# Performance work log

Measured on AMD Instinct MI355X. Metric: run time of the kernel, lower is better.

## Reference

```python
import jax, jax.numpy as jnp
import numpy as np

G = 8            # n_group
C = 256          # input_dim / channels
N_MEM = C // G   # 32
ALPHA = 0.4      # w_alpha
EPS = 1e-5
SLOPE = 0.01     # LeakyReLU negative slope


def _lrelu(x):
    return jnp.where(x >= 0, x, SLOPE * x)


def _mlp(x, ws, bs):
    # torch nn.Linear convention: y = x @ W.T + b; lrelu on all but last layer
    n = len(ws)
    for i in range(n):
        x = x @ ws[i].T + bs[i]
        if i < n - 1:
            x = _lrelu(x)
    return x


def _wct(c_A, s_B, mask, ct_ws, ct_bs, mu_ws, mu_bs):
    B, Cc, H, W = c_A.shape
    n_mem = Cc // G
    # style -> per-group coloring matrices  (Get.coloring, vectorized over groups)
    s_CT = _mlp(s_B.reshape(B * G, n_mem), ct_ws, ct_bs).reshape(B, G, n_mem, n_mem)
    D = jnp.sqrt(jnp.sum(s_CT ** 2, axis=2, keepdims=True))        # [B,G,1,n_mem]
    U = s_CT / D                                                    # column-normalized
    UDU = jnp.einsum('bgij,bgkj->bgik', s_CT, U)                    # [B,G,n_mem,n_mem]
    # torch.cat(U_arr, dim=0) is group-major: index g*B+b
    eigen_s = jnp.transpose(U, (1, 0, 2, 3)).reshape(G * B, n_mem, n_mem)
    X = jnp.tile(UDU.reshape(B, Cc, n_mem), (1, 1, G)) * mask       # [B,C,C]
    s_mu = _mlp(s_B, mu_ws, mu_bs)[:, :, None, None]                # [B,C,1,1]
    # per-group covariance of mean-centered content
    c_g = jnp.transpose(c_A, (1, 0, 2, 3)).reshape(G, n_mem, B * H * W)
    c_g = c_g - jnp.mean(c_g, axis=2, keepdims=True)
    cov_c = jnp.einsum('gin,gjn->gij', c_g, c_g) / (B * H * W - 1) \
        + EPS * jnp.eye(n_mem, dtype=c_A.dtype)
    # centered content, reinterpreted as [B, C, H*W] (matches torch view/permute)
    whitend = jnp.transpose(c_g.reshape(Cc, B, H * W), (1, 0, 2))
    colored = jnp.einsum('bcd,bdn->bcn', X, whitend).reshape(B, Cc, H, W)
    out = ALPHA * (colored + s_mu) + (1.0 - ALPHA) * c_A
    return out, cov_c, eigen_s


def setup_inputs():
    key = jax.random.key(0)
    ks = jax.random.split(key, 16)
    B, H, W = 4, 128, 128
    c_A = jax.random.normal(ks[0], (B, C, H, W), dtype=jnp.float32)
    s_B = jax.random.normal(ks[1], (B, C), dtype=jnp.float32)
    # block-diagonal group mask [1, C, C]
    m = np.zeros((C, C), dtype=np.float32)
    for g in range(G):
        m[g * N_MEM:(g + 1) * N_MEM, g * N_MEM:(g + 1) * N_MEM] = 1.0
    mask = jnp.asarray(m)[None]

    def lin(k, o, i):
        return jax.random.normal(k, (o, i), dtype=jnp.float32) * (1.0 / np.sqrt(i))

    inp = {'c_A': c_A, 's_B': s_B, 'mask': mask}
    dims_ct = [(256, 32), (256, 256), (256, 256), (256, 256), (1024, 256)]
    for j, (o, i) in enumerate(dims_ct):
        inp['ct_w%d' % j] = lin(ks[2 + j], o, i)
        inp['ct_b%d' % j] = jnp.zeros((o,), dtype=jnp.float32)
    dims_mu = [(256, 256), (256, 256), (256, 256)]
    for j, (o, i) in enumerate(dims_mu):
        inp['mu_w%d' % j] = lin(ks[8 + j], o, i)
        inp['mu_b%d' % j] = jnp.zeros((o,), dtype=jnp.float32)
    return inp


def reference(c_A, s_B, mask, ct_w0, ct_b0, ct_w1, ct_b1, ct_w2, ct_b2,
              ct_w3, ct_b3, ct_w4, ct_b4, mu_w0, mu_b0, mu_w1, mu_b1,
              mu_w2, mu_b2):
    ct_ws = (ct_w0, ct_w1, ct_w2, ct_w3, ct_w4)
    ct_bs = (ct_b0, ct_b1, ct_b2, ct_b3, ct_b4)
    mu_ws = (mu_w0, mu_w1, mu_w2)
    mu_bs = (mu_b0, mu_b1, mu_b2)
    return _wct(c_A, s_B, mask, ct_ws, ct_bs, mu_ws, mu_bs)
```

## Files before the change

### kernel.cpp

```cpp
#include <hip/hip_runtime.h>
#include <hip/hip_bf16.h>

typedef __bf16 bf16x8 __attribute__((ext_vector_type(8)));
typedef float  f32x16 __attribute__((ext_vector_type(16)));

#define ALPHA_W 0.4f
#define NTOT 65536.0f

#define OUT_MAIN 16777216
#define OUT_COV  (OUT_MAIN)
#define OUT_EIG  (OUT_MAIN + 8192)

#define WS_PSXY  0
#define WS_PSX   524288
#define WS_XA    540672
#define WS_XB    548864
#define WS_MUA   557056
#define WS_MUB   558080
#define WS_SMU   559104
#define WS_CT    560128
#define WS_M     592896
#define WS_T     625664

struct LJ { const float* X; const float* W; const float* B; float* Y; int act; int out; };

__device__ __forceinline__ float lrelu(float x) { return x >= 0.f ? x : 0.01f * x; }

__device__ __forceinline__ float dotg256(const float* __restrict__ w, const float* __restrict__ x) {
    float a0 = 0.f, a1 = 0.f, a2 = 0.f, a3 = 0.f;
    #pragma unroll
    for (int i = 0; i < 256; i += 16) {
        float4 w0 = *(const float4*)(w + i);
        float4 w1 = *(const float4*)(w + i + 4);
        float4 w2 = *(const float4*)(w + i + 8);
        float4 w3 = *(const float4*)(w + i + 12);
        float4 x0 = *(const float4*)(x + i);
        float4 x1 = *(const float4*)(x + i + 4);
        float4 x2 = *(const float4*)(x + i + 8);
        float4 x3 = *(const float4*)(x + i + 12);
        a0 = fmaf(w0.x, x0.x, a0); a0 = fmaf(w0.y, x0.y, a0);
        a0 = fmaf(w0.z, x0.z, a0); a0 = fmaf(w0.w, x0.w, a0);
        a1 = fmaf(w1.x, x1.x, a1); a1 = fmaf(w1.y, x1.y, a1);
        a1 = fmaf(w1.z, x1.z, a1); a1 = fmaf(w1.w, x1.w, a1);
        a2 = fmaf(w2.x, x2.x, a2); a2 = fmaf(w2.y, x2.y, a2);
        a2 = fmaf(w2.z, x2.z, a2); a2 = fmaf(w2.w, x2.w, a2);
        a3 = fmaf(w3.x, x3.x, a3); a3 = fmaf(w3.y, x3.y, a3);
        a3 = fmaf(w3.z, x3.z, a3); a3 = fmaf(w3.w, x3.w, a3);
    }
    return (a0 + a1) + (a2 + a3);
}

__global__ __launch_bounds__(256, 2) void gram_kernel(const float* __restrict__ cA,
                                                      float* __restrict__ pSXY,
                                                      float* __restrict__ pSX) {
    int bid = blockIdx.x;
    int g = bid >> 6, slice = bid & 63;
    int tid = threadIdx.x;
    int w = tid >> 6, l = tid & 63;
    int col = l & 31, kq = l >> 5;
    int nbase = slice * 1024 + w * 256;
    int b = nbase >> 14, hw0 = nbase & 16383;
    const float* base = cA + (((size_t)(b * 256 + g * 32 + col)) << 14) + hw0 + kq * 8;
    f32x16 acc;
    #pragma unroll
    for (int r = 0; r < 16; r++) acc[r] = 0.f;
    float s0 = 0.f, s1 = 0.f;
    #pragma unroll 8
    for (int it = 0; it < 16; ++it) {
        float4 f0 = *(const float4*)(base + it * 16);
        float4 f1 = *(const float4*)(base + it * 16 + 4);
        s0 += (f0.x + f0.y) + (f0.z + f0.w);
        s1 += (f1.x + f1.y) + (f1.z + f1.w);
        bf16x8 v;
        v[0] = (__bf16)f0.x; v[1] = (__bf16)f0.y; v[2] = (__bf16)f0.z; v[3] = (__bf16)f0.w;
        v[4] = (__bf16)f1.x; v[5] = (__bf16)f1.y; v[6] = (__bf16)f1.z; v[7] = (__bf16)f1.w;
        acc = __builtin_amdgcn_mfma_f32_32x32x16_bf16(v, v, acc, 0, 0, 0);
    }
    __shared__ float red[4][1024];
    __shared__ float sxr[4][64];
    sxr[w][l] = s0 + s1;
    #pragma unroll
    for (int r = 0; r < 16; r++) {
        int i = (r & 3) + 8 * (r >> 2) + 4 * kq;
        red[w][i * 32 + col] = acc[r];
    }
    __syncthreads();
    for (int e = tid; e < 1024; e += 256)
        pSXY[(size_t)bid * 1024 + e] = red[0][e] + red[1][e] + red[2][e] + red[3][e];
    if (tid < 32) {
        float v = 0.f;
        #pragma unroll
        for (int ww = 0; ww < 4; ww++) v += sxr[ww][tid] + sxr[ww][tid + 32];
        pSX[bid * 32 + tid] = v;
    }
}

__global__ __launch_bounds__(256, 2) void lin_first(const float* __restrict__ sB,
                                                    const float* __restrict__ w0,
                                                    const float* __restrict__ b0,
                                                    float* __restrict__ XA,
                                                    const float* __restrict__ mw0,
                                                    const float* __restrict__ mb0,
                                                    float* __restrict__ MUA) {
    int bid = blockIdx.x, tid = threadIdx.x;
    if (bid < 32) {
        __shared__ float xls[32 * 36];
        #pragma unroll
        for (int c = 0; c < 4; c++) {
            int idx = c * 256 + tid;
            xls[(idx >> 5) * 36 + (idx & 31)] = sB[idx];
        }
        __syncthreads();
        int o = bid * 8 + (tid & 7), r = tid >> 3;
        const float* wr = w0 + o * 32;
        const float* xr = xls + r * 36;
        float a0 = 0.f, a1 = 0.f;
        #pragma unroll
        for (int i = 0; i < 32; i += 8) {
            float4 u0 = *(const float4*)(wr + i);
            float4 u1 = *(const float4*)(wr + i + 4);
            float4 x0 = *(const float4*)(xr + i);
            float4 x1 = *(const float4*)(xr + i + 4);
            a0 = fmaf(u0.x, x0.x, a0); a0 = fmaf(u0.y, x0.y, a0);
            a0 = fmaf(u0.z, x0.z, a0); a0 = fmaf(u0.w, x0.w, a0);
            a1 = fmaf(u1.x, x1.x, a1); a1 = fmaf(u1.y, x1.y, a1);
            a1 = fmaf(u1.z, x1.z, a1); a1 = fmaf(u1.w, x1.w, a1);
        }
        XA[r * 256 + o] = lrelu(a0 + a1 + b0[o]);
    } else {
        __shared__ float xmu[4 * 260];
        {
            int idx = tid * 4;
            float4 v = *(const float4*)(sB + idx);
            *(float4*)(xmu + (idx >> 8) * 260 + (idx & 255)) = v;
        }
        __syncthreads();
        int o = (bid - 32) * 64 + (tid & 63), r = tid >> 6;
        float v = dotg256(mw0 + (size_t)o * 256, xmu + r * 260);
        MUA[r * 256 + o] = lrelu(v + mb0[o]);
    }
}

__global__ __launch_bounds__(256, 2) void lin256(LJ a, LJ b, int nbA) {
    int bid = blockIdx.x, tid = threadIdx.x;
    __shared__ float xls[32 * 260];
    if (bid < nbA) {
        #pragma unroll
        for (int c = 0; c < 8; c++) {
            int idx = c * 1024 + tid * 4;
            float4 v = *(const float4*)(a.X + idx);
            *(float4*)(xls + (idx >> 8) * 260 + (idx & 255)) = v;
        }
        __syncthreads();
        int o = bid * 8 + (tid & 7), r = tid >> 3;
        float v = dotg256(a.W + (size_t)o * 256, xls + r * 260) + a.B[o];
        a.Y[r * a.out + o] = a.act ? lrelu(v) : v;
    } else {
        {
            int idx = tid * 4;
            float4 v = *(const float4*)(b.X + idx);
            *(float4*)(xls + (idx >> 8) * 260 + (idx & 255)) = v;
        }
        __syncthreads();
        int o = (bid - nbA) * 64 + (tid & 63), r = tid >> 6;
        float v = dotg256(b.W + (size_t)o * 256, xls + r * 260) + b.B[o];
        b.Y[r * b.out + o] = b.act ? lrelu(v) : v;
    }
}

__global__ __launch_bounds__(256, 2) void finalize(const float* __restrict__ CT,
                                                   const float* __restrict__ SMU,
                                                   const float* __restrict__ pSXY,
                                                   const float* __restrict__ pSX,
                                                   float* __restrict__ M,
                                                   float* __restrict__ T,
                                                   float* __restrict__ out) {
    int bid = blockIdx.x, t = threadIdx.x;
    __shared__ float sxg[32];
    if (bid < 32) {
        int b = bid >> 3, g = bid & 7;
        __shared__ float sct[32 * 33], uu[32 * 33], ud[32 * 33], dinv[32];
        for (int e = t; e < 1024; e += 256) sct[(e >> 5) * 33 + (e & 31)] = CT[bid * 1024 + e];
        if (t < 32) {
            float s = 0.f;
            #pragma unroll
            for (int sl = 0; sl < 64; sl++) s += pSX[(g * 64 + sl) * 32 + t];
            sxg[t] = s * (1.0f / NTOT);
        }
        __syncthreads();
        if (t < 32) {
            float s = 0.f;
            #pragma unroll
            for (int i = 0; i < 32; i++) { float v = sct[i * 33 + t]; s = fmaf(v, v, s); }
            dinv[t] = 1.0f / sqrtf(s);
        }
        __syncthreads();
        float* eig = out + OUT_EIG + (size_t)(g * 4 + b) * 1024;
        for (int e = t; e < 1024; e += 256) {
            int i = e >> 5, jj = e & 31;
            float u = sct[i * 33 + jj] * dinv[jj];
            uu[i * 33 + jj] = u;
            eig[e] = u;
        }
        __syncthreads();
        float* Mo = M + (size_t)bid * 1024;
        for (int e = t; e < 1024; e += 256) {
            int i = e >> 5, k = e & 31;
            float s = 0.f;
            #pragma unroll
            for (int jv = 0; jv < 32; jv++) s = fmaf(sct[i * 33 + jv], uu[k * 33 + jv], s);
            ud[i * 33 + k] = s;
            Mo[e] = ALPHA_W * s + (i == k ? (1.0f - ALPHA_W) : 0.0f);
        }
        __syncthreads();
        if (t < 32) {
            float s = 0.f;
            #pragma unroll
            for (int k = 0; k < 32; k++) s = fmaf(ud[t * 33 + k], sxg[k], s);
            T[bid * 32 + t] = ALPHA_W * (SMU[bid * 32 + t] - s);
        }
    } else {
        int g = bid - 32;
        if (t < 32) {
            float s = 0.f;
            #pragma unroll
            for (int sl = 0; sl < 64; sl++) s += pSX[(g * 64 + sl) * 32 + t];
            sxg[t] = s * (1.0f / NTOT);
        }
        __syncthreads();
        float* cov = out + OUT_COV + (size_t)g * 1024;
        for (int e = t; e < 1024; e += 256) {
            float s = 0.f;
            #pragma unroll
            for (int sl = 0; sl < 64; sl++) s += pSXY[(size_t)(g * 64 + sl) * 1024 + e];
            int i = e >> 5, jj = e & 31;
            float vv = (s - NTOT * sxg[i] * sxg[jj]) * (1.0f / (NTOT - 1.0f));
            if (i == jj) vv += 1e-5f;
            cov[e] = vv;
        }
    }
}

__global__ __launch_bounds__(256) void color_kernel(const float* __restrict__ cA,
                                                    const float* __restrict__ M,
                                                    const float* __restrict__ T,
                                                    float* __restrict__ out) {
    int bid = blockIdx.x;
    int bg = bid >> 5, chunk = bid & 31;
    int b = bg >> 3, g = bg & 7;
    int tid = threadIdx.x;
    int n = tid & 63, ih = tid >> 6;
    __shared__ float Ml[1024];
    __shared__ float tl[32];
    __shared__ float xs[2][2048];
    for (int e = tid; e < 1024; e += 256) Ml[e] = M[(size_t)bg * 1024 + e];
    if (tid < 32) tl[tid] = T[bg * 32 + tid];
    size_t cbase = (((size_t)(b * 256 + g * 32)) << 14) + chunk * 512;
    int srow = tid >> 3, scol = (tid & 7) * 8;
    size_t obase = (((size_t)(b * 256 + g * 32 + ih * 8)) << 14) + chunk * 512 + n;
    for (int tile = 0; tile < 8; ++tile) {
        const float* src = cA + cbase + (size_t)srow * 16384 + tile * 64 + scol;
        float4 u0 = *(const float4*)src;
        float4 u1 = *(const float4*)(src + 4);
        float* xd = &xs[tile & 1][srow * 64 + scol];
        *(float4*)xd = u0;
        *(float4*)(xd + 4) = u1;
        __syncthreads();
        const float* xb = xs[tile & 1];
        float acc[8];
        #pragma unroll
        for (int i = 0; i < 8; i++) acc[i] = tl[ih * 8 + i];
        #pragma unroll
        for (int k = 0; k < 32; k++) {
            float xv = xb[k * 64 + n];
            #pragma unroll
            for (int i = 0; i < 8; i++) acc[i] = fmaf(Ml[(ih * 8 + i) * 32 + k], xv, acc[i]);
        }
        float* dst = out + obase + tile * 64;
        #pragma unroll
        for (int i = 0; i < 8; i++) dst[(size_t)i << 14] = acc[i];
    }
}

extern "C" void kernel_launch(void* const* d_in, const int* in_sizes, int n_in,
                              void* d_out, int out_size, void* d_ws, size_t ws_size,
                              hipStream_t stream) {
    (void)in_sizes; (void)n_in; (void)out_size; (void)ws_size;
    const float* cA = (const float*)d_in[0];
    const float* sB = (const float*)d_in[1];
    const float* ctw[5] = {(const float*)d_in[3], (const float*)d_in[5], (const float*)d_in[7],
                           (const float*)d_in[9], (const float*)d_in[11]};
    const float* ctb[5] = {(const float*)d_in[4], (const float*)d_in[6], (const float*)d_in[8],
                           (const float*)d_in[10], (const float*)d_in[12]};
    const float* muw[3] = {(const float*)d_in[13], (const float*)d_in[15], (const float*)d_in[17]};
    const float* mub[3] = {(const float*)d_in[14], (const float*)d_in[16], (const float*)d_in[18]};
    float* W = (float*)d_ws;
    float* out = (float*)d_out;

    gram_kernel<<<512, 256, 0, stream>>>(cA, W + WS_PSXY, W + WS_PSX);

    lin_first<<<36, 256, 0, stream>>>(sB, ctw[0], ctb[0], W + WS_XA, muw[0], mub[0], W + WS_MUA);
    LJ a, b;
    a = {W + WS_XA, ctw[1], ctb[1], W + WS_XB, 1, 256};
    b = {W + WS_MUA, muw[1], mub[1], W + WS_MUB, 1, 256};
    lin256<<<36, 256, 0, stream>>>(a, b, 32);
    a = {W + WS_XB, ctw[2], ctb[2], W + WS_XA, 1, 256};
    b = {W + WS_MUB, muw[2], mub[2], W + WS_SMU, 0, 256};
    lin256<<<36, 256, 0, stream>>>(a, b, 32);
    a = {W + WS_XA, ctw[3], ctb[3], W + WS_XB, 1, 256};
    lin256<<<32, 256, 0, stream>>>(a, a, 32);
    a = {W + WS_XB, ctw[4], ctb[4], W + WS_CT, 0, 1024};
    lin256<<<128, 256, 0, stream>>>(a, a, 128);

    finalize<<<40, 256, 0, stream>>>(W + WS_CT, W + WS_SMU, W + WS_PSXY, W + WS_PSX,
                                     W + WS_M, W + WS_T, out);
    color_kernel<<<1024, 256, 0, stream>>>(cA, W + WS_M, W + WS_T, out);
}
```

Measured before the change: 228.2 us.

## Fuse MLP chains into gram kernel and finalize into color kernel

After: 236.6 us. 1.04x slower.

```diff
diff --git a/kernel.cpp b/kernel.cpp
--- a/kernel.cpp
+++ b/kernel.cpp
@@ -13,16 +13,19 @@
 
 #define WS_PSXY  0
 #define WS_PSX   524288
-#define WS_XA    540672
-#define WS_XB    548864
-#define WS_MUA   557056
-#define WS_MUB   558080
 #define WS_SMU   559104
 #define WS_CT    560128
-#define WS_M     592896
-#define WS_T     625664
-
-struct LJ { const float* X; const float* W; const float* B; float* Y; int act; int out; };
+
+struct WP {
+    const float* cw0; const float* cb0;
+    const float* cw1; const float* cb1;
+    const float* cw2; const float* cb2;
+    const float* cw3; const float* cb3;
+    const float* cw4; const float* cb4;
+    const float* mw0; const float* mb0;
+    const float* mw1; const float* mb1;
+    const float* mw2; const float* mb2;
+};
 
 __device__ __forceinline__ float lrelu(float x) { return x >= 0.f ? x : 0.01f * x; }
 
@@ -50,12 +53,64 @@
     return (a0 + a1) + (a2 + a3);
 }
 
-__global__ __launch_bounds__(256, 2) void gram_kernel(const float* __restrict__ cA,
+__global__ __launch_bounds__(256, 2) void fused_front(const float* __restrict__ cA,
+                                                      const float* __restrict__ sB,
+                                                      WP wp,
                                                       float* __restrict__ pSXY,
-                                                      float* __restrict__ pSX) {
+                                                      float* __restrict__ pSX,
+                                                      float* __restrict__ CT,
+                                                      float* __restrict__ SMU) {
     int bid = blockIdx.x;
-    int g = bid >> 6, slice = bid & 63;
     int tid = threadIdx.x;
+    if (bid < 36) {
+        __shared__ float xb_[256], hb_[256];
+        int t = tid;
+        if (bid < 32) {
+            int r = bid;
+            if (t < 32) xb_[t] = sB[r * 32 + t];
+            __syncthreads();
+            {
+                const float* wr = wp.cw0 + t * 32;
+                float a0 = 0.f, a1 = 0.f;
+                #pragma unroll
+                for (int i = 0; i < 32; i += 8) {
+                    float4 u0 = *(const float4*)(wr + i);
+                    float4 u1 = *(const float4*)(wr + i + 4);
+                    float4 x0 = *(const float4*)(xb_ + i);
+                    float4 x1 = *(const float4*)(xb_ + i + 4);
+                    a0 = fmaf(u0.x, x0.x, a0); a0 = fmaf(u0.y, x0.y, a0);
+                    a0 = fmaf(u0.z, x0.z, a0); a0 = fmaf(u0.w, x0.w, a0);
+                    a1 = fmaf(u1.x, x1.x, a1); a1 = fmaf(u1.y, x1.y, a1);
+                    a1 = fmaf(u1.z, x1.z, a1); a1 = fmaf(u1.w, x1.w, a1);
+                }
+                hb_[t] = lrelu(a0 + a1 + wp.cb0[t]);
+            }
+            __syncthreads();
+            xb_[t] = lrelu(dotg256(wp.cw1 + (size_t)t * 256, hb_) + wp.cb1[t]);
+            __syncthreads();
+            hb_[t] = lrelu(dotg256(wp.cw2 + (size_t)t * 256, xb_) + wp.cb2[t]);
+            __syncthreads();
+            xb_[t] = lrelu(dotg256(wp.cw3 + (size_t)t * 256, hb_) + wp.cb3[t]);
+            __syncthreads();
+            #pragma unroll
+            for (int c = 0; c < 4; c++) {
+                int o = c * 256 + t;
+                CT[(size_t)r * 1024 + o] = dotg256(wp.cw4 + (size_t)o * 256, xb_) + wp.cb4[o];
+            }
+        } else {
+            int r = bid - 32;
+            xb_[t] = sB[r * 256 + t];
+            __syncthreads();
+            hb_[t] = lrelu(dotg256(wp.mw0 + (size_t)t * 256, xb_) + wp.mb0[t]);
+            __syncthreads();
+            xb_[t] = lrelu(dotg256(wp.mw1 + (size_t)t * 256, hb_) + wp.mb1[t]);
+            __syncthreads();
+            SMU[r * 256 + t] = dotg256(wp.mw2 + (size_t)t * 256, xb_) + wp.mb2[t];
+        }
+        return;
+    }
+    int gbid = bid - 36;
+    int g = gbid >> 6, slice = gbid & 63;
     int w = tid >> 6, l = tid & 63;
     int col = l & 31, kq = l >> 5;
     int nbase = slice * 1024 + w * 256;
@@ -86,150 +141,42 @@
     }
     __syncthreads();
     for (int e = tid; e < 1024; e += 256)
-        pSXY[(size_t)bid * 1024 + e] = red[0][e] + red[1][e] + red[2][e] + red[3][e];
+        pSXY[(size_t)gbid * 1024 + e] = red[0][e] + red[1][e] + red[2][e] + red[3][e];
     if (tid < 32) {
         float v = 0.f;
         #pragma unroll
         for (int ww = 0; ww < 4; ww++) v += sxr[ww][tid] + sxr[ww][tid + 32];
-        pSX[bid * 32 + tid] = v;
-    }
-}
-
-__global__ __launch_bounds__(256, 2) void lin_first(const float* __restrict__ sB,
-                                                    const float* __restrict__ w0,
-                                                    const float* __restrict__ b0,
-                                                    float* __restrict__ XA,
-                                                    const float* __restrict__ mw0,
-                                                    const float* __restrict__ mb0,
-                                                    float* __restrict__ MUA) {
-    int bid = blockIdx.x, tid = threadIdx.x;
-    if (bid < 32) {
-        __shared__ float xls[32 * 36];
-        #pragma unroll
-        for (int c = 0; c < 4; c++) {
-            int idx = c * 256 + tid;
-            xls[(idx >> 5) * 36 + (idx & 31)] = sB[idx];
-        }
-        __syncthreads();
-        int o = bid * 8 + (tid & 7), r = tid >> 3;
-        const float* wr = w0 + o * 32;
-        const float* xr = xls + r * 36;
-        float a0 = 0.f, a1 = 0.f;
-        #pragma unroll
-        for (int i = 0; i < 32; i += 8) {
-            float4 u0 = *(const float4*)(wr + i);
-            float4 u1 = *(const float4*)(wr + i + 4);
-            float4 x0 = *(const float4*)(xr + i);
-            float4 x1 = *(const float4*)(xr + i + 4);
-            a0 = fmaf(u0.x, x0.x, a0); a0 = fmaf(u0.y, x0.y, a0);
-            a0 = fmaf(u0.z, x0.z, a0); a0 = fmaf(u0.w, x0.w, a0);
-            a1 = fmaf(u1.x, x1.x, a1); a1 = fmaf(u1.y, x1.y, a1);
-            a1 = fmaf(u1.z, x1.z, a1); a1 = fmaf(u1.w, x1.w, a1);
-        }
-        XA[r * 256 + o] = lrelu(a0 + a1 + b0[o]);
-    } else {
-        __shared__ float xmu[4 * 260];
-        {
-            int idx = tid * 4;
-            float4 v = *(const float4*)(sB + idx);
-            *(float4*)(xmu + (idx >> 8) * 260 + (idx & 255)) = v;
-        }
-        __syncthreads();
-        int o = (bid - 32) * 64 + (tid & 63), r = tid >> 6;
-        float v = dotg256(mw0 + (size_t)o * 256, xmu + r * 260);
-        MUA[r * 256 + o] = lrelu(v + mb0[o]);
-    }
-}
-
-__global__ __launch_bounds__(256, 2) void lin256(LJ a, LJ b, int nbA) {
-    int bid = blockIdx.x, tid = threadIdx.x;
-    __shared__ float xls[32 * 260];
-    if (bid < nbA) {
-        #pragma unroll
-        for (int c = 0; c < 8; c++) {
-            int idx = c * 1024 + tid * 4;
-            float4 v = *(const float4*)(a.X + idx);
-            *(float4*)(xls + (idx >> 8) * 260 + (idx & 255)) = v;
-        }
-        __syncthreads();
-        int o = bid * 8 + (tid & 7), r = tid >> 3;
-        float v = dotg256(a.W + (size_t)o * 256, xls + r * 260) + a.B[o];
-        a.Y[r * a.out + o] = a.act ? lrelu(v) : v;
-    } else {
-        {
-            int idx = tid * 4;
-            float4 v = *(const float4*)(b.X + idx);
-            *(float4*)(xls + (idx >> 8) * 260 + (idx & 255)) = v;
-        }
-        __syncthreads();
-        int o = (bid - nbA) * 64 + (tid & 63), r = tid >> 6;
-        float v = dotg256(b.W + (size_t)o * 256, xls + r * 260) + b.B[o];
-        b.Y[r * b.out + o] = b.act ? lrelu(v) : v;
-    }
-}
-
-__global__ __launch_bounds__(256, 2) void finalize(const float* __restrict__ CT,
+        pSX[gbid * 32 + tid] = v;
+    }
+}
+
+__global__ __launch_bounds__(256) void color_fused(const float* __restrict__ cA,
+                                                   const float* __restrict__ CT,
                                                    const float* __restrict__ SMU,
+                                                   const float* __restrict__ pSX,
                                                    const float* __restrict__ pSXY,
-                                                   const float* __restrict__ pSX,
-                                                   float* __restrict__ M,
-                                                   float* __restrict__ T,
                                                    float* __restrict__ out) {
-    int bid = blockIdx.x, t = threadIdx.x;
+    __shared__ float sct[32 * 33];
+    __shared__ float sctd[32 * 33];
+    __shared__ float Ml[1024];
+    __shared__ float tl[32];
     __shared__ float sxg[32];
-    if (bid < 32) {
-        int b = bid >> 3, g = bid & 7;
-        __shared__ float sct[32 * 33], uu[32 * 33], ud[32 * 33], dinv[32];
-        for (int e = t; e < 1024; e += 256) sct[(e >> 5) * 33 + (e & 31)] = CT[bid * 1024 + e];
-        if (t < 32) {
+    __shared__ float dinv[32];
+    __shared__ float xs[2][2048];
+    int bid = blockIdx.x;
+    int tid = threadIdx.x;
+
+    if (bid >= 1024) {
+        int g = bid - 1024;
+        if (tid < 32) {
             float s = 0.f;
             #pragma unroll
-            for (int sl = 0; sl < 64; sl++) s += pSX[(g * 64 + sl) * 32 + t];
-            sxg[t] = s * (1.0f / NTOT);
-        }
-        __syncthreads();
-        if (t < 32) {
-            float s = 0.f;
-            #pragma unroll
-            for (int i = 0; i < 32; i++) { float v = sct[i * 33 + t]; s = fmaf(v, v, s); }
-            dinv[t] = 1.0f / sqrtf(s);
-        }
-        __syncthreads();
-        float* eig = out + OUT_EIG + (size_t)(g * 4 + b) * 1024;
-        for (int e = t; e < 1024; e += 256) {
-            int i = e >> 5, jj = e & 31;
-            float u = sct[i * 33 + jj] * dinv[jj];
-            uu[i * 33 + jj] = u;
-            eig[e] = u;
-        }
-        __syncthreads();
-        float* Mo = M + (size_t)bid * 1024;
-        for (int e = t; e < 1024; e += 256) {
-            int i = e >> 5, k = e & 31;
-            float s = 0.f;
-            #pragma unroll
-            for (int jv = 0; jv < 32; jv++) s = fmaf(sct[i * 33 + jv], uu[k * 33 + jv], s);
-            ud[i * 33 + k] = s;
-            Mo[e] = ALPHA_W * s + (i == k ? (1.0f - ALPHA_W) : 0.0f);
-        }
-        __syncthreads();
-        if (t < 32) {
-            float s = 0.f;
-            #pragma unroll
-            for (int k = 0; k < 32; k++) s = fmaf(ud[t * 33 + k], sxg[k], s);
-            T[bid * 32 + t] = ALPHA_W * (SMU[bid * 32 + t] - s);
-        }
-    } else {
-        int g = bid - 32;
-        if (t < 32) {
-            float s = 0.f;
-            #pragma unroll
-            for (int sl = 0; sl < 64; sl++) s += pSX[(g * 64 + sl) * 32 + t];
-            sxg[t] = s * (1.0f / NTOT);
+            for (int sl = 0; sl < 64; sl++) s += pSX[(g * 64 + sl) * 32 + tid];
+            sxg[tid] = s * (1.0f / NTOT);
         }
         __syncthreads();
         float* cov = out + OUT_COV + (size_t)g * 1024;
-        for (int e = t; e < 1024; e += 256) {
+        for (int e = tid; e < 1024; e += 256) {
             float s = 0.f;
             #pragma unroll
             for (int sl = 0; sl < 64; sl++) s += pSXY[(size_t)(g * 64 + sl) * 1024 + e];
@@ -238,23 +185,52 @@
             if (i == jj) vv += 1e-5f;
             cov[e] = vv;
         }
-    }
-}
-
-__global__ __launch_bounds__(256) void color_kernel(const float* __restrict__ cA,
-                                                    const float* __restrict__ M,
-                                                    const float* __restrict__ T,
-                                                    float* __restrict__ out) {
-    int bid = blockIdx.x;
+        return;
+    }
+
     int bg = bid >> 5, chunk = bid & 31;
     int b = bg >> 3, g = bg & 7;
-    int tid = threadIdx.x;
+
+    for (int e = tid; e < 1024; e += 256) sct[(e >> 5) * 33 + (e & 31)] = CT[(size_t)bg * 1024 + e];
+    if (tid < 32) {
+        float s = 0.f;
+        #pragma unroll
+        for (int sl = 0; sl < 64; sl++) s += pSX[(g * 64 + sl) * 32 + tid];
+        sxg[tid] = s * (1.0f / NTOT);
+    }
+    __syncthreads();
+    if (tid < 32) {
+        float s = 0.f;
+        #pragma unroll
+        for (int i = 0; i < 32; i++) { float v = sct[i * 33 + tid]; s = fmaf(v, v, s); }
+        dinv[tid] = 1.0f / sqrtf(s);
+    }
+    __syncthreads();
+    for (int e = tid; e < 1024; e += 256) {
+        int i = e >> 5, j = e & 31;
+        sctd[i * 33 + j] = sct[i * 33 + j] * dinv[j];
+    }
+    __syncthreads();
+    if (chunk == 0) {
+        float* eig = out + OUT_EIG + (size_t)(g * 4 + b) * 1024;
+        for (int e = tid; e < 1024; e += 256) eig[e] = sctd[(e >> 5) * 33 + (e & 31)];
+    }
+    for (int e = tid; e < 1024; e += 256) {
+        int i = e >> 5, k = e & 31;
+        float s = 0.f;
+        #pragma unroll
+        for (int j = 0; j < 32; j++) s = fmaf(sct[i * 33 + j], sctd[k * 33 + j], s);
+        Ml[e] = ALPHA_W * s + (i == k ? (1.0f - ALPHA_W) : 0.0f);
+    }
+    __syncthreads();
+    if (tid < 32) {
+        float s = 0.f;
+        #pragma unroll
+        for (int k = 0; k < 32; k++) s = fmaf(Ml[tid * 32 + k], sxg[k], s);
+        tl[tid] = ALPHA_W * SMU[bg * 32 + tid] - s + (1.0f - ALPHA_W) * sxg[tid];
+    }
+
     int n = tid & 63, ih = tid >> 6;
-    __shared__ float Ml[1024];
-    __shared__ float tl[32];
-    __shared__ float xs[2][2048];
-    for (int e = tid; e < 1024; e += 256) Ml[e] = M[(size_t)bg * 1024 + e];
-    if (tid < 32) tl[tid] = T[bg * 32 + tid];
     size_t cbase = (((size_t)(b * 256 + g * 32)) << 14) + chunk * 512;
     int srow = tid >> 3, scol = (tid & 7) * 8;
     size_t obase = (((size_t)(b * 256 + g * 32 + ih * 8)) << 14) + chunk * 512 + n;
@@ -288,31 +264,20 @@
     (void)in_sizes; (void)n_in; (void)out_size; (void)ws_size;
     const float* cA = (const float*)d_in[0];
     const float* sB = (const float*)d_in[1];
-    const float* ctw[5] = {(const float*)d_in[3], (const float*)d_in[5], (const float*)d_in[7],
-                           (const float*)d_in[9], (const float*)d_in[11]};
-    const float* ctb[5] = {(const float*)d_in[4], (const float*)d_in[6], (const float*)d_in[8],
-                           (const float*)d_in[10], (const float*)d_in[12]};
-    const float* muw[3] = {(const float*)d_in[13], (const float*)d_in[15], (const float*)d_in[17]};
-    const float* mub[3] = {(const float*)d_in[14], (const float*)d_in[16], (const float*)d_in[18]};
+    WP wp;
+    wp.cw0 = (const float*)d_in[3];  wp.cb0 = (const float*)d_in[4];
+    wp.cw1 = (const float*)d_in[5];  wp.cb1 = (const float*)d_in[6];
+    wp.cw2 = (const float*)d_in[7];  wp.cb2 = (const float*)d_in[8];
+    wp.cw3 = (const float*)d_in[9];  wp.cb3 = (const float*)d_in[10];
+    wp.cw4 = (const float*)d_in[11]; wp.cb4 = (const float*)d_in[12];
+    wp.mw0 = (const float*)d_in[13]; wp.mb0 = (const float*)d_in[14];
+    wp.mw1 = (const float*)d_in[15]; wp.mb1 = (const float*)d_in[16];
+    wp.mw2 = (const float*)d_in[17]; wp.mb2 = (const float*)d_in[18];
     float* W = (float*)d_ws;
     float* out = (float*)d_out;
 
-    gram_kernel<<<512, 256, 0, stream>>>(cA, W + WS_PSXY, W + WS_PSX);
-
-    lin_first<<<36, 256, 0, stream>>>(sB, ctw[0], ctb[0], W + WS_XA, muw[0], mub[0], W + WS_MUA);
-    LJ a, b;
-    a = {W + WS_XA, ctw[1], ctb[1], W + WS_XB, 1, 256};
-    b = {W + WS_MUA, muw[1], mub[1], W + WS_MUB, 1, 256};
-    lin256<<<36, 256, 0, stream>>>(a, b, 32);
-    a = {W + WS_XB, ctw[2], ctb[2], W + WS_XA, 1, 256};
-    b = {W + WS_MUB, muw[2], mub[2], W + WS_SMU, 0, 256};
-    lin256<<<36, 256, 0, stream>>>(a, b, 32);
-    a = {W + WS_XA, ctw[3], ctb[3], W + WS_XB, 1, 256};
-    lin256<<<32, 256, 0, stream>>>(a, a, 32);
-    a = {W + WS_XB, ctw[4], ctb[4], W + WS_CT, 0, 1024};
-    lin256<<<128, 256, 0, stream>>>(a, a, 128);
-
-    finalize<<<40, 256, 0, stream>>>(W + WS_CT, W + WS_SMU, W + WS_PSXY, W + WS_PSX,
-                                     W + WS_M, W + WS_T, out);
-    color_kernel<<<1024, 256, 0, stream>>>(cA, W + WS_M, W + WS_T, out);
-}
+    fused_front<<<548, 256, 0, stream>>>(cA, sB, wp, W + WS_PSXY, W + WS_PSX,
+                                         W + WS_CT, W + WS_SMU);
+    color_fused<<<1032, 256, 0, stream>>>(cA, W + WS_CT, W + WS_SMU,
+                                          W + WS_PSX, W + WS_PSXY, out);
+}
```
